# Optimization experiments

Measured on AMD Instinct MI355X. Metric: run time of the kernel, lower is better.

## Reference

```python
import jax, jax.numpy as jnp
import numpy as np

T, B, DIM = 64, 16, 512
H, Dh, ETA = 8, 64, 4
FD = ETA * Dh  # feature_dim = 256
EPS = 1e-6


def setup_inputs() -> dict:
    key = jax.random.key(0)
    ks = jax.random.split(key, 12)

    def w(k, o, i):
        return jax.random.normal(k, (o, i), jnp.float32) * (1.0 / np.sqrt(i).astype(np.float32))

    return {
        "inputs": jax.random.normal(ks[0], (T, B, DIM), jnp.float32),
        "terminations": jax.random.randint(ks[1], (T, B), 0, 2).astype(jnp.int32),
        "kv_state_prev": jnp.zeros((B, H, FD, Dh), jnp.float32),
        "norm_state_prev": jnp.zeros((B, H, FD), jnp.float32),
        "Wq": w(ks[2], H * Dh, DIM),
        "Wk": w(ks[3], H * Dh, DIM),
        "Wv": w(ks[4], H * Dh, DIM),
        "Wb": w(ks[5], H * Dh, DIM),
        "Wg": w(ks[6], H * Dh, DIM),
        "Wp1": w(ks[7], H * ETA, DIM),
        "Wp2": w(ks[8], H * ETA, DIM),
        "Wp3": w(ks[9], H * ETA, DIM),
        "Wo": w(ks[10], DIM, H * Dh),
        "bo": jnp.zeros((DIM,), jnp.float32),
    }


def reference(inputs, terminations, kv_state_prev, norm_state_prev,
              Wq, Wk, Wv, Wb, Wg, Wp1, Wp2, Wp3, Wo, bo):
    def proj(W, e):
        return (inputs @ W.T).reshape(T, B, H, e)

    q = proj(Wq, Dh)
    k = proj(Wk, Dh)
    v = proj(Wv, Dh)
    beta = jax.nn.sigmoid(proj(Wb, Dh))
    gamma = jax.nn.sigmoid(proj(Wg, Dh))
    p1 = proj(Wp1, ETA)
    p2 = proj(Wp2, ETA)
    p3 = proj(Wp3, ETA)

    # feature map: outer product of relu(p) [eta] and x [head_dim] -> [eta*head_dim]
    def fmap(x, p):
        return jnp.einsum('tbhe,tbhd->tbhed', jax.nn.relu(p), x).reshape(T, B, H, FD)

    phi_q = fmap(q, p2)
    psi_k = fmap(k, p1)
    # gamma map: outer product of sigmoid(p3) and sigmoid-gated gamma, values in (0,1)
    gamma_feat = jnp.einsum('tbhe,tbhd->tbhed', jax.nn.sigmoid(p3), gamma).reshape(T, B, H, FD)

    gated_v = v * beta                       # [T,B,H,Dh]
    gated_k = psi_k * gamma_feat             # [T,B,H,FD]

    term_mask = (1.0 - terminations.astype(jnp.float32))[:, :, None, None]  # [T,B,1,1]
    discount = (1.0 - gamma_feat) * term_mask  # [T,B,H,FD]

    kv_upd = jnp.einsum('tbhd,tbhD->tbhDd', gated_v, gated_k)  # [T,B,H,FD,Dh]

    def step(carry, x):
        kv, nm = carry
        d, u_kv, u_nm = x
        kv = d[..., None] * kv + u_kv
        nm = d * nm + u_nm
        return (kv, nm), (kv, nm)

    _, (kv_all, nm_all) = jax.lax.scan(step, (kv_state_prev, norm_state_prev),
                                       (discount, kv_upd, gated_k))

    attn_num = jnp.einsum('tbhDd,tbhD->tbhd', kv_all, phi_q)
    attn_den = jnp.einsum('tbhD,tbhD->tbh', phi_q, nm_all)
    attn_out = (attn_num / (attn_den[..., None] + EPS)).reshape(T, B, H * Dh)
    output = attn_out @ Wo.T + bo
    return (output, kv_all[-1], nm_all[-1])
```

## Files before the change

### kernel.cpp

```cpp
#include <hip/hip_runtime.h>


#define T_N   64
#define B_N   16
#define DIM_N 512
#define H_N   8
#define DH_N  64

#define OUT_ELEMS   524288
#define KV_ELEMS    2097152
#define PROJ_ELEMS  2719744

typedef _Float16 f16;
typedef f16   f16x8 __attribute__((ext_vector_type(8)));
typedef float f32x4 __attribute__((ext_vector_type(4)));

__device__ __forceinline__ float sigmoidf_(float x) {
    return 1.0f / (1.0f + __expf(-x));
}

template <int CTRL, int RM>
__device__ __forceinline__ float dpp_add_(float x) {
    int mv = __builtin_amdgcn_update_dpp(__float_as_int(x), __float_as_int(x),
                                         CTRL, RM, 0xF, false);
    return x + __int_as_float(mv);
}
__device__ __forceinline__ float half_reduce_dpp(float x) {
    x = dpp_add_<0xB1, 0xF>(x);
    x = dpp_add_<0x4E, 0xF>(x);
    x = dpp_add_<0x141, 0xF>(x);
    x = dpp_add_<0x140, 0xF>(x);
    x = dpp_add_<0x142, 0xA>(x);
    return x;
}

__device__ __forceinline__ void cvt_split_store(f16* __restrict__ dh,
                                                f16* __restrict__ dl,
                                                float4 v0, float4 v1) {
    float x[8] = {v0.x, v0.y, v0.z, v0.w, v1.x, v1.y, v1.z, v1.w};
    f16x8 h, lo;
    #pragma unroll
    for (int e = 0; e < 8; ++e) {
        f16 hh = (f16)x[e];
        h[e]  = hh;
        lo[e] = (f16)(x[e] - (float)hh);
    }
    *(f16x8*)dh = h;
    *(f16x8*)dl = lo;
}

__device__ __forceinline__ void mfma64_core(const float* __restrict__ A,
                                            const float* __restrict__ W,
                                            const float* __restrict__ bias,
                                            float* __restrict__ C, int N,
                                            int mb, int nb) {
    const int nbase = nb * 64;
    if (nbase >= N) return;
    const int mbase = mb * 64;

    __shared__ f16 AsH[2][64][40];
    __shared__ f16 AsL[2][64][40];
    __shared__ f16 BsH[2][64][40];
    __shared__ f16 BsL[2][64][40];

    const int tid = threadIdx.x;
    const int sr = tid >> 2;
    const int kq = (tid & 3) << 3;
    const bool wok = (nbase + sr) < N;
    const float* Ap = A + (size_t)(mbase + sr) * 512 + kq;
    const float* Wp = W + (size_t)(nbase + sr) * 512 + kq;

    const int l  = tid & 63;
    const int w  = tid >> 6;
    const int wr = (w >> 1) << 5;
    const int wc = (w & 1) << 5;
    const int lr = l & 15;
    const int lk = (l >> 4) << 3;

    f32x4 acc[2][2] = {};

    float4 xa0 = *(const float4*)(Ap);
    float4 xa1 = *(const float4*)(Ap + 4);
    float4 wb0 = wok ? *(const float4*)(Wp)     : make_float4(0.f, 0.f, 0.f, 0.f);
    float4 wb1 = wok ? *(const float4*)(Wp + 4) : make_float4(0.f, 0.f, 0.f, 0.f);
    cvt_split_store(&AsH[0][sr][kq], &AsL[0][sr][kq], xa0, xa1);
    cvt_split_store(&BsH[0][sr][kq], &BsL[0][sr][kq], wb0, wb1);

    for (int k0 = 0; k0 < 512; k0 += 32) {
        const int buf = (k0 >> 5) & 1;
        __syncthreads();
        const bool more = (k0 + 32) < 512;
        if (more) {
            xa0 = *(const float4*)(Ap + k0 + 32);
            xa1 = *(const float4*)(Ap + k0 + 36);
            wb0 = wok ? *(const float4*)(Wp + k0 + 32) : make_float4(0.f, 0.f, 0.f, 0.f);
            wb1 = wok ? *(const float4*)(Wp + k0 + 36) : make_float4(0.f, 0.f, 0.f, 0.f);
        }

        f16x8 aH[2], aL[2], bH[2], bL[2];
        #pragma unroll
        for (int i = 0; i < 2; ++i) {
            const int row = wr + i * 16 + lr;
            aH[i] = *(const f16x8*)&AsH[buf][row][lk];
            aL[i] = *(const f16x8*)&AsL[buf][row][lk];
        }
        #pragma unroll
        for (int j = 0; j < 2; ++j) {
            const int col = wc + j * 16 + lr;
            bH[j] = *(const f16x8*)&BsH[buf][col][lk];
            bL[j] = *(const f16x8*)&BsL[buf][col][lk];
        }

        #pragma unroll
        for (int i = 0; i < 2; ++i)
            #pragma unroll
            for (int j = 0; j < 2; ++j) {
                acc[i][j] = __builtin_amdgcn_mfma_f32_16x16x32_f16(aH[i], bH[j], acc[i][j], 0, 0, 0);
                acc[i][j] = __builtin_amdgcn_mfma_f32_16x16x32_f16(aH[i], bL[j], acc[i][j], 0, 0, 0);
                acc[i][j] = __builtin_amdgcn_mfma_f32_16x16x32_f16(aL[i], bH[j], acc[i][j], 0, 0, 0);
            }

        if (more) {
            const int nbuf = buf ^ 1;
            cvt_split_store(&AsH[nbuf][sr][kq], &AsL[nbuf][sr][kq], xa0, xa1);
            cvt_split_store(&BsH[nbuf][sr][kq], &BsL[nbuf][sr][kq], wb0, wb1);
        }
    }

    #pragma unroll
    for (int j = 0; j < 2; ++j) {
        const int n = nbase + wc + j * 16 + lr;
        if (n < N) {
            const float bv = bias ? bias[n] : 0.f;
            #pragma unroll
            for (int i = 0; i < 2; ++i) {
                #pragma unroll
                for (int q = 0; q < 4; ++q) {
                    const int m = mbase + wr + i * 16 + ((l >> 4) << 2) + q;
                    C[(size_t)m * N + n] = acc[i][j][q] + bv;
                }
            }
        }
    }
}

struct ProjW {
    const float* W[8];
    float*       D[8];
};

__global__ __launch_bounds__(256) void proj_mfma_kernel(const float* __restrict__ X,
                                                        ProjW a) {
    const int id = blockIdx.x;
    const int z = id & 7;
    const int rem = id >> 3;
    const int mb = rem & 15;
    const int nb = rem >> 4;
    const int N = (z < 5) ? 512 : 32;
    mfma64_core(X, a.W[z], nullptr, a.D[z], N, mb, nb);
}

__global__ __launch_bounds__(256) void out_mfma_kernel(const float* __restrict__ A,
                                                       const float* __restrict__ W,
                                                       const float* __restrict__ bias,
                                                       float* __restrict__ C) {
    const int id = blockIdx.x;
    const int mb = id & 15;
    const int nb = id >> 4;
    mfma64_core(A, W, bias, C, 512, mb, nb);
}

__global__ __launch_bounds__(256) void gate_kernel(
    const float* __restrict__ qb,  const float* __restrict__ kb,
    const float* __restrict__ vb,  const float* __restrict__ bb,
    const float* __restrict__ gb,  const float* __restrict__ p1b,
    const float* __restrict__ p2b, const float* __restrict__ p3b,
    const int* __restrict__ term,
    float* __restrict__ disc_g, float* __restrict__ gk_g,
    float* __restrict__ phiq_g, float* __restrict__ gv_g) {
    const int h = blockIdx.x;
    const int row = blockIdx.y;
    const int D = threadIdx.x;
    const int e = D >> 6, di = D & 63;
    const size_t base = (size_t)row * 512 + h * 64;
    const size_t pb = (size_t)row * 32 + h * 4;

    float q = qb[base + di], k = kb[base + di], g = gb[base + di];
    float p1 = p1b[pb + e], p2 = p2b[pb + e], p3 = p3b[pb + e];
    float mask = 1.0f - (float)term[row];
    float gf = sigmoidf_(p3) * sigmoidf_(g);

    const size_t o = ((size_t)row * 8 + h) * 256 + D;
    disc_g[o] = (1.0f - gf) * mask;
    gk_g[o]   = fmaxf(p1, 0.f) * k * gf;
    phiq_g[o] = fmaxf(p2, 0.f) * q;
    if (D < 64)
        gv_g[((size_t)row * 8 + h) * 64 + D] = vb[base + D] * sigmoidf_(bb[base + D]);
}

__global__ __launch_bounds__(256) void scan8_kernel(
    const float* __restrict__ disc_g, const float* __restrict__ gk_g,
    const float* __restrict__ phiq_g, const float* __restrict__ gv_g,
    float* __restrict__ vb ,
    const float* __restrict__ kv0, const float* __restrict__ nm0,
    float* __restrict__ dout) {
    const int blk = blockIdx.x;
    const int bh = blk & 127;
    const int s  = blk >> 7;
    const int b  = bh >> 3;
    const int h  = bh & 7;
    const int tid = threadIdx.x;
    const int w = tid >> 6;
    const int l = tid & 63;
    const int half = l >> 5;
    const int li = l & 31;
    const int d0 = s * 16 + w * 4 + half * 2;
    const int D0 = li << 3;

    float kv[8][2];
    float nm[8];
    {
        const float* kp = kv0 + ((size_t)bh * 256 + D0) * 64 + d0;
        #pragma unroll
        for (int j = 0; j < 8; ++j) {
            float2 r = *(const float2*)(kp + (size_t)j * 64);
            kv[j][0] = r.x; kv[j][1] = r.y;
        }
        float4 na  = *(const float4*)(nm0 + (size_t)bh * 256 + D0);
        float4 nb_ = *(const float4*)(nm0 + (size_t)bh * 256 + D0 + 4);
        nm[0] = na.x; nm[1] = na.y; nm[2] = na.z; nm[3] = na.w;
        nm[4] = nb_.x; nm[5] = nb_.y; nm[6] = nb_.z; nm[7] = nb_.w;
    }

    float4 cd0, cd1, cg0, cg1, cp0, cp1; float2 cgv;
    {
        const size_t go = ((size_t)b * 8 + h) * 256 + D0;
        cd0 = *(const float4*)(disc_g + go);  cd1 = *(const float4*)(disc_g + go + 4);
        cg0 = *(const float4*)(gk_g + go);    cg1 = *(const float4*)(gk_g + go + 4);
        cp0 = *(const float4*)(phiq_g + go);  cp1 = *(const float4*)(phiq_g + go + 4);
        cgv = *(const float2*)(gv_g + ((size_t)b * 8 + h) * 64 + d0);
    }

    for (int t = 0; t < T_N; ++t) {
        const int row = t * B_N + b;
        const size_t base = (size_t)row * 512 + h * 64;

        float4 nd0 = {}, nd1 = {}, ng0 = {}, ng1 = {}, np0 = {}, np1 = {};
        float2 ngv = {};
        if (t + 1 < T_N) {
            const size_t go2 = ((size_t)(row + B_N) * 8 + h) * 256 + D0;
            nd0 = *(const float4*)(disc_g + go2); nd1 = *(const float4*)(disc_g + go2 + 4);
            ng0 = *(const float4*)(gk_g + go2);   ng1 = *(const float4*)(gk_g + go2 + 4);
            np0 = *(const float4*)(phiq_g + go2); np1 = *(const float4*)(phiq_g + go2 + 4);
            ngv = *(const float2*)(gv_g + ((size_t)(row + B_N) * 8 + h) * 64 + d0);
        }

        const float dj[8]  = {cd0.x, cd0.y, cd0.z, cd0.w, cd1.x, cd1.y, cd1.z, cd1.w};
        const float gkj[8] = {cg0.x, cg0.y, cg0.z, cg0.w, cg1.x, cg1.y, cg1.z, cg1.w};
        const float phj[8] = {cp0.x, cp0.y, cp0.z, cp0.w, cp1.x, cp1.y, cp1.z, cp1.w};

        float den = 0.f, n0 = 0.f, n1 = 0.f;
        #pragma unroll
        for (int j = 0; j < 8; ++j) {
            nm[j] = dj[j] * nm[j] + gkj[j];
            den = fmaf(phj[j], nm[j], den);
            kv[j][0] = dj[j] * kv[j][0] + gkj[j] * cgv.x; n0 = fmaf(phj[j], kv[j][0], n0);
            kv[j][1] = dj[j] * kv[j][1] + gkj[j] * cgv.y; n1 = fmaf(phj[j], kv[j][1], n1);
        }

        n0  = half_reduce_dpp(n0);
        n1  = half_reduce_dpp(n1);
        den = half_reduce_dpp(den);

        if (li == 16) {
            vb[base + d0]     = n0 / (den + 1e-6f);
            vb[base + d0 + 1] = n1 / (den + 1e-6f);
        }

        cd0 = nd0; cd1 = nd1; cg0 = ng0; cg1 = ng1; cp0 = np0; cp1 = np1; cgv = ngv;
    }

    {
        float* kp = dout + OUT_ELEMS + ((size_t)bh * 256 + D0) * 64 + d0;
        #pragma unroll
        for (int j = 0; j < 8; ++j)
            *(float2*)(kp + (size_t)j * 64) = make_float2(kv[j][0], kv[j][1]);
        if (s == 0 && w == 0 && half == 0) {
            float* np = dout + OUT_ELEMS + KV_ELEMS + (size_t)bh * 256 + D0;
            *(float4*)np       = make_float4(nm[0], nm[1], nm[2], nm[3]);
            *(float4*)(np + 4) = make_float4(nm[4], nm[5], nm[6], nm[7]);
        }
    }
}

extern "C" void kernel_launch(void* const* d_in, const int* in_sizes, int n_in,
                              void* d_out, int out_size, void* d_ws, size_t ws_size,
                              hipStream_t stream) {
    (void)in_sizes; (void)n_in; (void)out_size;

    const float* X    = (const float*)d_in[0];
    const int*   term = (const int*)  d_in[1];
    const float* kv0  = (const float*)d_in[2];
    const float* nm0  = (const float*)d_in[3];
    const float* Wo   = (const float*)d_in[12];
    const float* bo   = (const float*)d_in[13];

    float* out = (float*)d_out;

    float* qb  = (float*)d_ws;
    float* kb  = qb  + 524288;
    float* vb  = kb  + 524288;
    float* bb  = vb  + 524288;
    float* gb  = bb  + 524288;
    float* p1b = gb  + 524288;
    float* p2b = p1b + 32768;
    float* p3b = p2b + 32768;
    float* disc_g = p3b + 32768;
    float* gk_g   = disc_g + 2097152;
    float* phiq_g = gk_g   + 2097152;
    float* gv_g   = phiq_g + 2097152;

    ProjW pa;
    pa.W[0] = (const float*)d_in[4];  pa.W[1] = (const float*)d_in[5];
    pa.W[2] = (const float*)d_in[6];  pa.W[3] = (const float*)d_in[7];
    pa.W[4] = (const float*)d_in[8];  pa.W[5] = (const float*)d_in[9];
    pa.W[6] = (const float*)d_in[10]; pa.W[7] = (const float*)d_in[11];
    pa.D[0] = qb;  pa.D[1] = kb;  pa.D[2] = vb;  pa.D[3] = bb;
    pa.D[4] = gb;  pa.D[5] = p1b; pa.D[6] = p2b; pa.D[7] = p3b;
    proj_mfma_kernel<<<1024, 256, 0, stream>>>(X, pa);

    gate_kernel<<<dim3(8, 1024), 256, 0, stream>>>(qb, kb, vb, bb, gb,
                                                   p1b, p2b, p3b, term,
                                                   disc_g, gk_g, phiq_g, gv_g);
    scan8_kernel<<<512, 256, 0, stream>>>(disc_g, gk_g, phiq_g, gv_g,
                                          vb, kv0, nm0, out);
    out_mfma_kernel<<<128, 256, 0, stream>>>(vb, Wo, bo, out);
}
```

Measured before the change: 177.4 us.

## Fuse gating into scan kernel, recomputing features from raw projections

The separate gate kernel, which wrote expanded 256-wide discount, gated-key and phi-q tensors to global memory, is removed. The scan kernel now reads the raw q/k/g/v/beta/p projections and computes sigmoid, relu and the feature products in registers each time step. This drops a kernel launch and several MB of intermediate writes and reads. In exchange every scan block does extra sigmoid work inside the serial time loop, and the blocks split across d0 recompute the same features redundantly.

```diff
diff --git a/kernel.cpp b/kernel.cpp
--- a/kernel.cpp
+++ b/kernel.cpp
@@ -170,38 +170,13 @@
     mfma64_core(A, W, bias, C, 512, mb, nb);
 }
 
-__global__ __launch_bounds__(256) void gate_kernel(
-    const float* __restrict__ qb,  const float* __restrict__ kb,
-    const float* __restrict__ vb,  const float* __restrict__ bb,
-    const float* __restrict__ gb,  const float* __restrict__ p1b,
+__global__ __launch_bounds__(256) void scan12_kernel(
+    const float* __restrict__ qb, const float* __restrict__ kb,
+    const float* __restrict__ vbi, const float* __restrict__ bb,
+    const float* __restrict__ gb, const float* __restrict__ p1b,
     const float* __restrict__ p2b, const float* __restrict__ p3b,
     const int* __restrict__ term,
-    float* __restrict__ disc_g, float* __restrict__ gk_g,
-    float* __restrict__ phiq_g, float* __restrict__ gv_g) {
-    const int h = blockIdx.x;
-    const int row = blockIdx.y;
-    const int D = threadIdx.x;
-    const int e = D >> 6, di = D & 63;
-    const size_t base = (size_t)row * 512 + h * 64;
-    const size_t pb = (size_t)row * 32 + h * 4;
-
-    float q = qb[base + di], k = kb[base + di], g = gb[base + di];
-    float p1 = p1b[pb + e], p2 = p2b[pb + e], p3 = p3b[pb + e];
-    float mask = 1.0f - (float)term[row];
-    float gf = sigmoidf_(p3) * sigmoidf_(g);
-
-    const size_t o = ((size_t)row * 8 + h) * 256 + D;
-    disc_g[o] = (1.0f - gf) * mask;
-    gk_g[o]   = fmaxf(p1, 0.f) * k * gf;
-    phiq_g[o] = fmaxf(p2, 0.f) * q;
-    if (D < 64)
-        gv_g[((size_t)row * 8 + h) * 64 + D] = vb[base + D] * sigmoidf_(bb[base + D]);
-}
-
-__global__ __launch_bounds__(256) void scan8_kernel(
-    const float* __restrict__ disc_g, const float* __restrict__ gk_g,
-    const float* __restrict__ phiq_g, const float* __restrict__ gv_g,
-    float* __restrict__ vb ,
+    float* __restrict__ attn,
     const float* __restrict__ kv0, const float* __restrict__ nm0,
     float* __restrict__ dout) {
     const int blk = blockIdx.x;
@@ -216,6 +191,8 @@
     const int li = l & 31;
     const int d0 = s * 16 + w * 4 + half * 2;
     const int D0 = li << 3;
+    const int di0 = (D0 & 63);
+    const int e   = D0 >> 6;
 
     float kv[8][2];
     float nm[8];
@@ -232,40 +209,64 @@
         nm[4] = nb_.x; nm[5] = nb_.y; nm[6] = nb_.z; nm[7] = nb_.w;
     }
 
-    float4 cd0, cd1, cg0, cg1, cp0, cp1; float2 cgv;
+    float4 ck0, ck1, cg0, cg1, cq0, cq1;
+    float  cp1, cp2, cp3, cmask;
+    float2 cvv, cbb;
+
     {
-        const size_t go = ((size_t)b * 8 + h) * 256 + D0;
-        cd0 = *(const float4*)(disc_g + go);  cd1 = *(const float4*)(disc_g + go + 4);
-        cg0 = *(const float4*)(gk_g + go);    cg1 = *(const float4*)(gk_g + go + 4);
-        cp0 = *(const float4*)(phiq_g + go);  cp1 = *(const float4*)(phiq_g + go + 4);
-        cgv = *(const float2*)(gv_g + ((size_t)b * 8 + h) * 64 + d0);
+        const size_t base = (size_t)b * 512 + h * 64;
+        const size_t pb = (size_t)b * 32 + h * 4 + e;
+        ck0 = *(const float4*)(kb + base + di0); ck1 = *(const float4*)(kb + base + di0 + 4);
+        cg0 = *(const float4*)(gb + base + di0); cg1 = *(const float4*)(gb + base + di0 + 4);
+        cq0 = *(const float4*)(qb + base + di0); cq1 = *(const float4*)(qb + base + di0 + 4);
+        cp1 = p1b[pb]; cp2 = p2b[pb]; cp3 = p3b[pb];
+        cmask = 1.0f - (float)term[b];
+        cvv = *(const float2*)(vbi + base + d0);
+        cbb = *(const float2*)(bb + base + d0);
     }
 
     for (int t = 0; t < T_N; ++t) {
         const int row = t * B_N + b;
-        const size_t base = (size_t)row * 512 + h * 64;
-
-        float4 nd0 = {}, nd1 = {}, ng0 = {}, ng1 = {}, np0 = {}, np1 = {};
-        float2 ngv = {};
+
+        float4 nk0 = {}, nk1 = {}, ng0 = {}, ng1 = {}, nq0 = {}, nq1 = {};
+        float  np1 = 0.f, np2 = 0.f, np3 = 0.f, nmask = 0.f;
+        float2 nvv = {}, nbb = {};
         if (t + 1 < T_N) {
-            const size_t go2 = ((size_t)(row + B_N) * 8 + h) * 256 + D0;
-            nd0 = *(const float4*)(disc_g + go2); nd1 = *(const float4*)(disc_g + go2 + 4);
-            ng0 = *(const float4*)(gk_g + go2);   ng1 = *(const float4*)(gk_g + go2 + 4);
-            np0 = *(const float4*)(phiq_g + go2); np1 = *(const float4*)(phiq_g + go2 + 4);
-            ngv = *(const float2*)(gv_g + ((size_t)(row + B_N) * 8 + h) * 64 + d0);
-        }
-
-        const float dj[8]  = {cd0.x, cd0.y, cd0.z, cd0.w, cd1.x, cd1.y, cd1.z, cd1.w};
-        const float gkj[8] = {cg0.x, cg0.y, cg0.z, cg0.w, cg1.x, cg1.y, cg1.z, cg1.w};
-        const float phj[8] = {cp0.x, cp0.y, cp0.z, cp0.w, cp1.x, cp1.y, cp1.z, cp1.w};
+            const size_t nbase = (size_t)(row + B_N) * 512 + h * 64;
+            const size_t npb = (size_t)(row + B_N) * 32 + h * 4 + e;
+            nk0 = *(const float4*)(kb + nbase + di0); nk1 = *(const float4*)(kb + nbase + di0 + 4);
+            ng0 = *(const float4*)(gb + nbase + di0); ng1 = *(const float4*)(gb + nbase + di0 + 4);
+            nq0 = *(const float4*)(qb + nbase + di0); nq1 = *(const float4*)(qb + nbase + di0 + 4);
+            np1 = p1b[npb]; np2 = p2b[npb]; np3 = p3b[npb];
+            nmask = 1.0f - (float)term[row + B_N];
+            nvv = *(const float2*)(vbi + nbase + d0);
+            nbb = *(const float2*)(bb + nbase + d0);
+        }
+
+        const float kj[8] = {ck0.x, ck0.y, ck0.z, ck0.w, ck1.x, ck1.y, ck1.z, ck1.w};
+        const float gj[8] = {cg0.x, cg0.y, cg0.z, cg0.w, cg1.x, cg1.y, cg1.z, cg1.w};
+        const float qj[8] = {cq0.x, cq0.y, cq0.z, cq0.w, cq1.x, cq1.y, cq1.z, cq1.w};
+        const float sp3 = sigmoidf_(cp3);
+        const float r1 = fmaxf(cp1, 0.f);
+        const float r2 = fmaxf(cp2, 0.f);
+        float dj[8], gkj[8], phj[8];
+        #pragma unroll
+        for (int j = 0; j < 8; ++j) {
+            const float gf = sp3 * sigmoidf_(gj[j]);
+            dj[j]  = (1.0f - gf) * cmask;
+            gkj[j] = r1 * kj[j] * gf;
+            phj[j] = r2 * qj[j];
+        }
+        const float gvx = cvv.x * sigmoidf_(cbb.x);
+        const float gvy = cvv.y * sigmoidf_(cbb.y);
 
         float den = 0.f, n0 = 0.f, n1 = 0.f;
         #pragma unroll
         for (int j = 0; j < 8; ++j) {
             nm[j] = dj[j] * nm[j] + gkj[j];
             den = fmaf(phj[j], nm[j], den);
-            kv[j][0] = dj[j] * kv[j][0] + gkj[j] * cgv.x; n0 = fmaf(phj[j], kv[j][0], n0);
-            kv[j][1] = dj[j] * kv[j][1] + gkj[j] * cgv.y; n1 = fmaf(phj[j], kv[j][1], n1);
+            kv[j][0] = dj[j] * kv[j][0] + gkj[j] * gvx; n0 = fmaf(phj[j], kv[j][0], n0);
+            kv[j][1] = dj[j] * kv[j][1] + gkj[j] * gvy; n1 = fmaf(phj[j], kv[j][1], n1);
         }
 
         n0  = half_reduce_dpp(n0);
@@ -273,11 +274,13 @@
         den = half_reduce_dpp(den);
 
         if (li == 16) {
-            vb[base + d0]     = n0 / (den + 1e-6f);
-            vb[base + d0 + 1] = n1 / (den + 1e-6f);
-        }
-
-        cd0 = nd0; cd1 = nd1; cg0 = ng0; cg1 = ng1; cp0 = np0; cp1 = np1; cgv = ngv;
+            const size_t obase = (size_t)row * 512 + h * 64;
+            attn[obase + d0]     = n0 / (den + 1e-6f);
+            attn[obase + d0 + 1] = n1 / (den + 1e-6f);
+        }
+
+        ck0 = nk0; ck1 = nk1; cg0 = ng0; cg1 = ng1; cq0 = nq0; cq1 = nq1;
+        cp1 = np1; cp2 = np2; cp3 = np3; cmask = nmask; cvv = nvv; cbb = nbb;
     }
 
     {
@@ -296,7 +299,7 @@
 extern "C" void kernel_launch(void* const* d_in, const int* in_sizes, int n_in,
                               void* d_out, int out_size, void* d_ws, size_t ws_size,
                               hipStream_t stream) {
-    (void)in_sizes; (void)n_in; (void)out_size;
+    (void)in_sizes; (void)n_in; (void)out_size; (void)ws_size;
 
     const float* X    = (const float*)d_in[0];
     const int*   term = (const int*)  d_in[1];
@@ -315,10 +318,7 @@
     float* p1b = gb  + 524288;
     float* p2b = p1b + 32768;
     float* p3b = p2b + 32768;
-    float* disc_g = p3b + 32768;
-    float* gk_g   = disc_g + 2097152;
-    float* phiq_g = gk_g   + 2097152;
-    float* gv_g   = phiq_g + 2097152;
+    float* attn = p3b + 32768;
 
     ProjW pa;
     pa.W[0] = (const float*)d_in[4];  pa.W[1] = (const float*)d_in[5];
@@ -329,10 +329,9 @@
     pa.D[4] = gb;  pa.D[5] = p1b; pa.D[6] = p2b; pa.D[7] = p3b;
     proj_mfma_kernel<<<1024, 256, 0, stream>>>(X, pa);
 
-    gate_kernel<<<dim3(8, 1024), 256, 0, stream>>>(qb, kb, vb, bb, gb,
-                                                   p1b, p2b, p3b, term,
-                                                   disc_g, gk_g, phiq_g, gv_g);
-    scan8_kernel<<<512, 256, 0, stream>>>(disc_g, gk_g, phiq_g, gv_g,
-                                          vb, kv0, nm0, out);
-    out_mfma_kernel<<<128, 256, 0, stream>>>(vb, Wo, bo, out);
-}
+    scan12_kernel<<<512, 256, 0, stream>>>(qb, kb, vb, bb, gb,
+                                           p1b, p2b, p3b, term,
+                                           attn, kv0, nm0, out);
+
+    out_mfma_kernel<<<128, 256, 0, stream>>>(attn, Wo, bo, out);
+}
```

After: 225.1 us. +26.9%, slower.
